# Performance work log

Measured on AMD Instinct MI355X. Metric: run time of the kernel, lower is better.

Reference implementation:

```python
import jax, jax.numpy as jnp
import numpy as np

H, KVH, DH = 16, 4, 64
DIM = 1024
SCALE_BASE = 4096  # context_len
EPS = 1e-6


def rmsnorm(x, g):
    return x * jax.lax.rsqrt(jnp.mean(x * x, axis=-1, keepdims=True) + EPS) * g


def rope_tables(n, dh, dtype):
    inv_freq = 1.0 / (10000.0 ** (jnp.arange(0, dh, 2, dtype=jnp.float32) / dh))
    t = jnp.arange(n, dtype=jnp.float32) * (SCALE_BASE / n)
    freqs = t[:, None] * inv_freq[None, :]          # [n, dh/2]
    emb = jnp.concatenate([freqs, freqs], axis=-1)  # [n, dh]
    return jnp.cos(emb).astype(dtype), jnp.sin(emb).astype(dtype)


def apply_rope(x, cos, sin):
    # x: [b, h, n, dh]; cos/sin: [n, dh]
    x1, x2 = jnp.split(x, 2, axis=-1)
    rot = jnp.concatenate([-x2, x1], axis=-1)
    return x * cos + rot * sin


def setup_inputs() -> dict:
    key = jax.random.key(0)
    ks = jax.random.split(key, 12)
    B, N = 1, 2048
    std = 0.02
    inp = {
        "x": jax.random.normal(ks[0], (B, N, DIM), jnp.float32),
        "a": jax.random.normal(ks[1], (B, N, DIM), jnp.float32),
        "g_x": jnp.ones((DIM,), jnp.float32),
        "g_a": jnp.ones((DIM,), jnp.float32),
        "Wq_x": jax.random.normal(ks[2], (DIM, H * DH), jnp.float32) * std,
        "Wkv_x": jax.random.normal(ks[3], (DIM, 2 * KVH * DH), jnp.float32) * std,
        "Wq_a": jax.random.normal(ks[4], (DIM, H * DH), jnp.float32) * std,
        "Wkv_a": jax.random.normal(ks[5], (DIM, 2 * KVH * DH), jnp.float32) * std,
        "Wout_x": jax.random.normal(ks[6], (H * DH, DIM), jnp.float32) * std,
        "bout_x": jnp.zeros((DIM,), jnp.float32),
        "Wout_a": jax.random.normal(ks[7], (H * DH, DIM), jnp.float32) * std,
        "bout_a": jnp.zeros((DIM,), jnp.float32),
    }
    return inp


def _split_heads(t, h):
    b, n, hd = t.shape
    return t.reshape(b, n, h, hd // h).transpose(0, 2, 1, 3)  # b h n d


def _stream_qkv(s, g, Wq, Wkv):
    s = rmsnorm(s, g)
    q = _split_heads(s @ Wq, H)                 # [b, H, n, DH]
    kv = s @ Wkv
    k, v = jnp.split(kv, 2, axis=-1)
    k = _split_heads(k, KVH)                    # [b, KVH, n, DH]
    v = _split_heads(v, KVH)
    return q, k, v


def reference(x, a, g_x, g_a, Wq_x, Wkv_x, Wq_a, Wkv_a, Wout_x, bout_x, Wout_a, bout_a):
    B, Nx, _ = x.shape
    Na = a.shape[1]
    scale = DH ** -0.5
    r = H // KVH

    q_x, k_x, v_x = _stream_qkv(x, g_x, Wq_x, Wkv_x)
    q_a, k_a, v_a = _stream_qkv(a, g_a, Wq_a, Wkv_a)

    cos_x, sin_x = rope_tables(Nx, DH, x.dtype)
    cos_a, sin_a = rope_tables(Na, DH, a.dtype)
    q_x, k_x = apply_rope(q_x, cos_x, sin_x), apply_rope(k_x, cos_x, sin_x)
    q_a, k_a = apply_rope(q_a, cos_a, sin_a), apply_rope(k_a, cos_a, sin_a)

    # NOTE: original scales q by dim_head**-0.5 AND sdpa scales again -> 1/DH total
    q_x = q_x * scale
    q_a = q_a * scale

    # GQA expansion: einops 'b h n d -> b (r h) n d' == tile heads
    tile = lambda t: jnp.tile(t, (1, r, 1, 1))
    k_x, v_x, k_a, v_a = tile(k_x), tile(v_x), tile(k_a), tile(v_a)

    # pack [a, x] along seq
    q = jnp.concatenate([q_a, q_x], axis=2)
    k = jnp.concatenate([k_a, k_x], axis=2)
    v = jnp.concatenate([v_a, v_x], axis=2)

    scores = jnp.einsum('bhqd,bhkd->bhqk', q, k) * scale  # sdpa's own scale
    attn = jax.nn.softmax(scores, axis=-1)
    out = jnp.einsum('bhqk,bhkd->bhqd', attn, v)          # [b, H, Na+Nx, DH]

    out_a, out_x = out[:, :, :Na], out[:, :, Na:]
    merge = lambda t: t.transpose(0, 2, 1, 3).reshape(B, -1, H * DH)
    out_x = merge(out_x) @ Wout_x + bout_x
    out_a = merge(out_a) @ Wout_a + bout_a
    return out_x, out_a
```

## Files before the change

### kernel.cpp

```cpp
#include <hip/hip_runtime.h>
#include <hip/hip_bf16.h>
#include <stdint.h>
#include <math.h>


#define NSEQ 2048
#define NJ   4096
#define DIMM 1024

typedef __attribute__((ext_vector_type(4))) float f32x4;
typedef __attribute__((ext_vector_type(8))) short bf16x8;
typedef __attribute__((ext_vector_type(4))) short bf16x4;

__device__ __forceinline__ unsigned short f2bf(float f) {
  union { float f; uint32_t u; } v; v.f = f;
  return (unsigned short)((v.u + 0x7FFFu + ((v.u >> 16) & 1u)) >> 16);
}

__device__ __forceinline__ uint32_t pack2bf(float a, float b) {
  __hip_bfloat162 h = __float22bfloat162_rn(float2{a, b});
  union { __hip_bfloat162 h; uint32_t u; } c; c.h = h;
  return c.u;
}

#if defined(__has_builtin)
#if __has_builtin(__builtin_amdgcn_exp2f)
#define FAST_EXP2(x) __builtin_amdgcn_exp2f(x)
#endif
#endif
#ifndef FAST_EXP2
#define FAST_EXP2(x) exp2f(x)
#endif

__device__ __forceinline__ void glds16(const void* g, void* l) {
  __builtin_amdgcn_global_load_lds(
      (const __attribute__((address_space(1))) unsigned int*)g,
      (__attribute__((address_space(3))) unsigned int*)l, 16, 0, 0);
}

#define SYNC_VM(N) do {                                                    \
    asm volatile("s_waitcnt vmcnt(" #N ")" ::: "memory");                  \
    __builtin_amdgcn_sched_barrier(0);                                     \
    __builtin_amdgcn_s_barrier();                                          \
    __builtin_amdgcn_sched_barrier(0);                                     \
  } while (0)

__global__ __launch_bounds__(256) void prep_kernel(
    const float* __restrict__ xa, const float* __restrict__ xx,
    const float* __restrict__ ga, const float* __restrict__ gx,
    const float* __restrict__ wqa, const float* __restrict__ wqx,
    const float* __restrict__ wkva, const float* __restrict__ wkvx,
    const float* __restrict__ woa, const float* __restrict__ wox,
    unsigned short* __restrict__ XN, unsigned short* __restrict__ WQT,
    unsigned short* __restrict__ WKVT, unsigned short* __restrict__ WOT,
    float* __restrict__ cosT, float* __restrict__ sinT) {
  __shared__ float tile[32][33];
  __shared__ float red[4];
  int bid = blockIdx.x, t = threadIdx.x;
  if (bid < 256) {
    int idx = bid * 256 + t;
    int pos = idx >> 5, i = idx & 31;
    double inv = 1.0;
    if (i & 1)  inv *= 0.74989420933245582;
    if (i & 2)  inv *= 0.56234132519034908;
    if (i & 4)  inv *= 0.31622776601683794;
    if (i & 8)  inv *= 0.1;
    if (i & 16) inv *= 0.01;
    double ang = (double)(2 * pos) * inv;
    double rev = ang * 0.15915494309189535;
    rev -= floor(rev);
    float rf = (float)rev;
    float c, s;
    asm("v_cos_f32 %0, %1" : "=v"(c) : "v"(rf));
    asm("v_sin_f32 %0, %1" : "=v"(s) : "v"(rf));
    cosT[idx] = c;
    sinT[idx] = s;
  } else if (bid < 6400) {
    int b = bid - 256;
    int z = b >> 10, yx = b & 1023;
    int n0 = (yx >> 5) * 32, k0 = (yx & 31) * 32;
    int s = z & 1, ty = z >> 1;
    int N = (ty == 1) ? 512 : 1024;
    if (n0 >= N) return;
    const float* src = (z == 0) ? wqa : (z == 1) ? wqx : (z == 2) ? wkva
                     : (z == 3) ? wkvx : (z == 4) ? woa : wox;
    unsigned short* dst = (ty == 0) ? WQT + (size_t)s * 1024 * 1024
                        : (ty == 1) ? WKVT + (size_t)s * 512 * 1024
                                    : WOT + (size_t)s * 1024 * 1024;
    int r = t >> 3, c4 = (t & 7) * 4;
    f32x4 v = *(const f32x4*)(src + (size_t)(k0 + r) * N + n0 + c4);
    tile[r][c4 + 0] = v.x; tile[r][c4 + 1] = v.y;
    tile[r][c4 + 2] = v.z; tile[r][c4 + 3] = v.w;
    __syncthreads();
    int nn = t >> 3, kk = (t & 7) * 4;
    bf16x4 o;
    o.x = (short)f2bf(tile[kk + 0][nn]);
    o.y = (short)f2bf(tile[kk + 1][nn]);
    o.z = (short)f2bf(tile[kk + 2][nn]);
    o.w = (short)f2bf(tile[kk + 3][nn]);
    *(bf16x4*)(dst + (size_t)(n0 + nn) * 1024 + k0 + kk) = o;
  } else {
    int b = bid - 6400;
    int s = b >> 11, row = b & 2047;
    const float* src = (s == 0 ? xa : xx) + (size_t)row * DIMM;
    const float* g = (s == 0 ? ga : gx);
    f32x4 v = *(const f32x4*)(src + t * 4);
    float ss = v.x * v.x + v.y * v.y + v.z * v.z + v.w * v.w;
#pragma unroll
    for (int o = 32; o > 0; o >>= 1) ss += __shfl_xor(ss, o, 64);
    if ((t & 63) == 0) red[t >> 6] = ss;
    __syncthreads();
    float tot = red[0] + red[1] + red[2] + red[3];
    float rs = rsqrtf(tot * (1.0f / DIMM) + 1e-6f);
    f32x4 gv = *(const f32x4*)(g + t * 4);
    bf16x4 o;
    o.x = (short)f2bf(v.x * rs * gv.x);
    o.y = (short)f2bf(v.y * rs * gv.y);
    o.z = (short)f2bf(v.z * rs * gv.z);
    o.w = (short)f2bf(v.w * rs * gv.w);
    *(bf16x4*)(XN + ((size_t)s * NSEQ + row) * DIMM + t * 4) = o;
  }
}

__device__ __forceinline__ void gemm64_mainloop(
    const unsigned short* __restrict__ Ag, const unsigned short* __restrict__ Bg,
    unsigned short* As, unsigned short* Bs, f32x4 acc[2][4]) {
  int t = threadIdx.x;
  int lane = t & 63, wid = t >> 6;
  int wm = (wid >> 1) * 32, wn = (wid & 1) * 64;
  int l15 = lane & 15, quad = lane >> 4;
  int srow = t >> 2, sko = (t & 3) * 8;
  const unsigned short* ga = Ag + (size_t)srow * 1024 + sko;
  const unsigned short* gb = Bg + (size_t)srow * 1024 + sko;
  unsigned short* la = As + t * 8;
  unsigned short* lb = Bs + t * 8;
#pragma unroll
  for (int mi = 0; mi < 2; ++mi)
#pragma unroll
    for (int j = 0; j < 4; ++j) acc[mi][j] = (f32x4){0.f, 0.f, 0.f, 0.f};

#define GQ_STAGE(S, KT) do {                                               \
    int k0_ = (KT) * 32;                                                   \
    glds16(ga + k0_, la + (S) * 2048);                                     \
    glds16(gb + k0_, lb + (S) * 4096);                                     \
    glds16(gb + 64 * 1024 + k0_, lb + (S) * 4096 + 2048);                  \
  } while (0)

#define GQ_COMP(S) do {                                                    \
    bf16x8 af[2], bfr[4];                                                  \
    _Pragma("unroll")                                                      \
    for (int mi = 0; mi < 2; ++mi)                                         \
      af[mi] = *(const bf16x8*)(As + (S) * 2048 + (wm + mi * 16 + l15) * 32 + quad * 8); \
    _Pragma("unroll")                                                      \
    for (int j = 0; j < 4; ++j)                                            \
      bfr[j] = *(const bf16x8*)(Bs + (S) * 4096 + (wn + j * 16 + l15) * 32 + quad * 8); \
    _Pragma("unroll")                                                      \
    for (int mi = 0; mi < 2; ++mi)                                         \
      _Pragma("unroll")                                                    \
      for (int j = 0; j < 4; ++j)                                          \
        acc[mi][j] = __builtin_amdgcn_mfma_f32_16x16x32_bf16(af[mi], bfr[j], acc[mi][j], 0, 0, 0); \
  } while (0)

  GQ_STAGE(0, 0);
  GQ_STAGE(1, 1);
  SYNC_VM(3);
  for (int kq = 0; kq < 32; kq += 4) {
    GQ_STAGE(2, (kq + 2) & 31);
    GQ_COMP(0);
    SYNC_VM(3);
    GQ_STAGE(3, (kq + 3) & 31);
    GQ_COMP(1);
    SYNC_VM(3);
    GQ_STAGE(0, (kq + 4) & 31);
    GQ_COMP(2);
    SYNC_VM(3);
    GQ_STAGE(1, (kq + 5) & 31);
    GQ_COMP(3);
    SYNC_VM(3);
  }
  asm volatile("s_waitcnt vmcnt(0)" ::: "memory");
#undef GQ_STAGE
#undef GQ_COMP
}

__global__ __launch_bounds__(256) void gemm_qkv_kernel(
    const unsigned short* __restrict__ XN, const unsigned short* __restrict__ WQT,
    const unsigned short* __restrict__ WKVT, const float* __restrict__ cosT,
    const float* __restrict__ sinT, unsigned short* __restrict__ QB,
    unsigned short* __restrict__ KB, unsigned short* __restrict__ VT) {
  __shared__ unsigned short As[4 * 2048], Bs[4 * 4096];
  int n0 = blockIdx.x * 128, m0 = blockIdx.y * 64;
  int s = (m0 >= 2048) ? 1 : 0;
  const unsigned short* Ag = XN + (size_t)m0 * 1024;
  const unsigned short* Bg = (n0 < 1024)
      ? WQT + (size_t)s * 1024 * 1024 + (size_t)n0 * 1024
      : WKVT + (size_t)s * 512 * 1024 + (size_t)(n0 - 1024) * 1024;
  f32x4 acc[2][4];
  gemm64_mainloop(Ag, Bg, As, Bs, acc);
  int t = threadIdx.x, lane = t & 63, wid = t >> 6;
  int wm = (wid >> 1) * 32, wn = (wid & 1) * 64;
  int l15 = lane & 15, quad = lane >> 4;
  int coln = n0 + wn;
  if (coln < 1280) {
    bool isq = coln < 1024;
    float sc = isq ? (1.4426950408889634f / 64.0f) : 1.0f;
    unsigned short* dstBase;
    if (isq) dstBase = QB + (size_t)(coln >> 6) * NJ * 64;
    else     dstBase = KB + (size_t)((coln - 1024) >> 6) * NJ * 64;
#pragma unroll
    for (int mi = 0; mi < 2; ++mi)
#pragma unroll
      for (int r = 0; r < 4; ++r) {
        int jr = m0 + wm + mi * 16 + quad * 4 + r;
        int pos = jr & 2047;
#pragma unroll
        for (int jp = 0; jp < 2; ++jp) {
          int i = jp * 16 + l15;
          float c = cosT[pos * 32 + i], sn = sinT[pos * 32 + i];
          float x1 = acc[mi][jp][r], x2 = acc[mi][jp + 2][r];
          dstBase[(size_t)jr * 64 + jp * 16 + l15]      = f2bf((x1 * c - x2 * sn) * sc);
          dstBase[(size_t)jr * 64 + 32 + jp * 16 + l15] = f2bf((x2 * c + x1 * sn) * sc);
        }
      }
  } else {
    int cvb = coln - 1280;
#pragma unroll
    for (int mi = 0; mi < 2; ++mi)
#pragma unroll
      for (int j = 0; j < 4; ++j) {
        int d = cvb + j * 16 + l15;
        int jr0 = m0 + wm + mi * 16 + quad * 4;
        union { bf16x4 v; uint32_t u[2]; } pv;
        pv.u[0] = pack2bf(acc[mi][j][0], acc[mi][j][1]);
        pv.u[1] = pack2bf(acc[mi][j][2], acc[mi][j][3]);
        *(bf16x4*)(VT + (size_t)d * NJ + jr0) = pv.v;
      }
  }
}

__global__ __launch_bounds__(256, 2) void attn_kernel(
    const unsigned short* __restrict__ QB, const unsigned short* __restrict__ KB,
    const unsigned short* __restrict__ VT, unsigned short* __restrict__ AT) {
  __shared__ __align__(16) unsigned short Ks[4][4096];
  __shared__ __align__(16) unsigned short Vs[4][4096];
  int h = blockIdx.y, qt = blockIdx.x;
  int hk = h & 3;
  int t = threadIdx.x, lane = t & 63, w = t >> 6;
  int l15 = lane & 15, quad = lane >> 4;
  int qsel = w >> 1, ksel = w & 1;
  int q0 = qt * 128 + qsel * 64;
  bf16x8 qf[4][2];
#pragma unroll
  for (int mi = 0; mi < 4; ++mi) {
    const unsigned short* qp = QB + ((size_t)h * NJ + q0 + mi * 16 + l15) * 64;
    qf[mi][0] = *(const bf16x8*)(qp + quad * 8);
    qf[mi][1] = *(const bf16x8*)(qp + 32 + quad * 8);
  }
  f32x4 oT[4][4];
  f32x4 oL[4];
#pragma unroll
  for (int mi = 0; mi < 4; ++mi) {
    oL[mi] = (f32x4){0.f, 0.f, 0.f, 0.f};
#pragma unroll
    for (int db = 0; db < 4; ++db) oT[mi][db] = (f32x4){0.f, 0.f, 0.f, 0.f};
  }
  bf16x8 vone;
  {
    short one = (l15 == 0) ? (short)0x3F80 : (short)0;
    vone = (bf16x8){one, one, one, one, one, one, one, one};
  }
  const unsigned short* Kg = KB + (size_t)hk * NJ * 64;
  const unsigned short* Vg = VT + (size_t)hk * 64 * NJ;
  int r1 = t >> 3, cx = t & 7;
  int e1 = r1 & 7;
  int c1 = cx ^ e1;
  int gk1 = 32 * (r1 >> 5) + 8 * ((r1 >> 2) & 3) + 4 * ((r1 >> 4) & 1) + (r1 & 3);
  int r2 = r1 + 32;
  int gk2 = 32 * (r2 >> 5) + 8 * ((r2 >> 2) & 3) + 4 * ((r2 >> 4) & 1) + (r2 & 3);
  const unsigned short* sK1 = Kg + (size_t)gk1 * 64 + c1 * 8;
  const unsigned short* sK2 = Kg + (size_t)gk2 * 64 + c1 * 8;
  const unsigned short* sV1 = Vg + (size_t)r1 * NJ + c1 * 8;
  const unsigned short* sV2 = Vg + (size_t)r2 * NJ + c1 * 8;
  int e = l15 & 7;
  int co0 = (quad ^ e) * 8;
  int co1 = ((4 + quad) ^ e) * 8;
  int cov = (((ksel << 2) | quad) ^ e) * 8;
  const unsigned short* kf0p = &Ks[0][(2 * ksel * 16 + l15) * 64] + co0;
  const unsigned short* kf0q = &Ks[0][(2 * ksel * 16 + l15) * 64] + co1;
  const unsigned short* kf1p = kf0p + 16 * 64;
  const unsigned short* kf1q = kf0q + 16 * 64;
  const unsigned short* vap0 = &Vs[0][(0 * 16 + l15) * 64] + cov;
  const unsigned short* vap1 = &Vs[0][(1 * 16 + l15) * 64] + cov;
  const unsigned short* vap2 = &Vs[0][(2 * 16 + l15) * 64] + cov;
  const unsigned short* vap3 = &Vs[0][(3 * 16 + l15) * 64] + cov;

  f32x4 sxA[4][2], sxB[4][2];
  bf16x8 pb[4];

#define STAGE(S, T) do {                                                   \
    size_t ko_ = (size_t)(T) * 4096;                                       \
    int vo_ = (T) * 64;                                                    \
    glds16(sK1 + ko_, &Ks[S][0] + t * 8);                                  \
    glds16(sK2 + ko_, &Ks[S][2048] + t * 8);                               \
    glds16(sV1 + vo_, &Vs[S][0] + t * 8);                                  \
    glds16(sV2 + vo_, &Vs[S][2048] + t * 8);                               \
  } while (0)

#define QK4(S, SX) do {                                                    \
    bf16x8 k00 = *(const bf16x8*)(kf0p + (S) * 4096);                      \
    bf16x8 k01 = *(const bf16x8*)(kf0q + (S) * 4096);                      \
    bf16x8 k10 = *(const bf16x8*)(kf1p + (S) * 4096);                      \
    bf16x8 k11 = *(const bf16x8*)(kf1q + (S) * 4096);                      \
    _Pragma("unroll")                                                      \
    for (int mi = 0; mi < 4; ++mi) {                                       \
      f32x4 z0 = (f32x4){0.f, 0.f, 0.f, 0.f};                              \
      z0 = __builtin_amdgcn_mfma_f32_16x16x32_bf16(k00, qf[mi][0], z0, 0, 0, 0); \
      z0 = __builtin_amdgcn_mfma_f32_16x16x32_bf16(k01, qf[mi][1], z0, 0, 0, 0); \
      (SX)[mi][0] = z0;                                                    \
      f32x4 z1 = (f32x4){0.f, 0.f, 0.f, 0.f};                              \
      z1 = __builtin_amdgcn_mfma_f32_16x16x32_bf16(k10, qf[mi][0], z1, 0, 0, 0); \
      z1 = __builtin_amdgcn_mfma_f32_16x16x32_bf16(k11, qf[mi][1], z1, 0, 0, 0); \
      (SX)[mi][1] = z1;                                                    \
    }                                                                      \
  } while (0)

#define PHASE_A(SQ, SXN, SXP) do {                                         \
    bf16x8 k00 = *(const bf16x8*)(kf0p + (SQ) * 4096);                     \
    bf16x8 k01 = *(const bf16x8*)(kf0q + (SQ) * 4096);                     \
    bf16x8 k10 = *(const bf16x8*)(kf1p + (SQ) * 4096);                     \
    bf16x8 k11 = *(const bf16x8*)(kf1q + (SQ) * 4096);                     \
    _Pragma("unroll")                                                      \
    for (int mi = 0; mi < 4; ++mi) {                                       \
      f32x4 z0 = (f32x4){0.f, 0.f, 0.f, 0.f};                              \
      z0 = __builtin_amdgcn_mfma_f32_16x16x32_bf16(k00, qf[mi][0], z0, 0, 0, 0); \
      z0 = __builtin_amdgcn_mfma_f32_16x16x32_bf16(k01, qf[mi][1], z0, 0, 0, 0); \
      (SXN)[mi][0] = z0;                                                   \
      f32x4 z1 = (f32x4){0.f, 0.f, 0.f, 0.f};                              \
      z1 = __builtin_amdgcn_mfma_f32_16x16x32_bf16(k10, qf[mi][0], z1, 0, 0, 0); \
      z1 = __builtin_amdgcn_mfma_f32_16x16x32_bf16(k11, qf[mi][1], z1, 0, 0, 0); \
      (SXN)[mi][1] = z1;                                                   \
      union { bf16x8 v; uint32_t u[4]; } pk_;                              \
      pk_.u[0] = pack2bf(FAST_EXP2((SXP)[mi][0][0]), FAST_EXP2((SXP)[mi][0][1])); \
      pk_.u[1] = pack2bf(FAST_EXP2((SXP)[mi][0][2]), FAST_EXP2((SXP)[mi][0][3])); \
      pk_.u[2] = pack2bf(FAST_EXP2((SXP)[mi][1][0]), FAST_EXP2((SXP)[mi][1][1])); \
      pk_.u[3] = pack2bf(FAST_EXP2((SXP)[mi][1][2]), FAST_EXP2((SXP)[mi][1][3])); \
      pb[mi] = pk_.v;                                                      \
    }                                                                      \
  } while (0)

#define PHASE_B(SP) do {                                                   \
    __builtin_amdgcn_s_setprio(1);                                         \
    {                                                                      \
      bf16x8 va0 = *(const bf16x8*)(vap0 + (SP) * 4096);                   \
      bf16x8 va1 = *(const bf16x8*)(vap1 + (SP) * 4096);                   \
      bf16x8 va2 = *(const bf16x8*)(vap2 + (SP) * 4096);                   \
      bf16x8 va3 = *(const bf16x8*)(vap3 + (SP) * 4096);                   \
      _Pragma("unroll")                                                    \
      for (int mi = 0; mi < 4; ++mi) {                                     \
        oT[mi][0] = __builtin_amdgcn_mfma_f32_16x16x32_bf16(va0, pb[mi], oT[mi][0], 0, 0, 0); \
        oT[mi][1] = __builtin_amdgcn_mfma_f32_16x16x32_bf16(va1, pb[mi], oT[mi][1], 0, 0, 0); \
        oT[mi][2] = __builtin_amdgcn_mfma_f32_16x16x32_bf16(va2, pb[mi], oT[mi][2], 0, 0, 0); \
        oT[mi][3] = __builtin_amdgcn_mfma_f32_16x16x32_bf16(va3, pb[mi], oT[mi][3], 0, 0, 0); \
        oL[mi] = __builtin_amdgcn_mfma_f32_16x16x32_bf16(vone, pb[mi], oL[mi], 0, 0, 0); \
      }                                                                    \
    }                                                                      \
    __builtin_amdgcn_s_setprio(0);                                         \
  } while (0)

  STAGE(0, 0);
  STAGE(1, 1);
  STAGE(2, 2);
  SYNC_VM(4);
  QK4(0, sxA);
  for (int P = 0; P < 16; ++P) {
    int tb = 4 * P;
    STAGE(3, (tb + 3) & 63);
    PHASE_A(1, sxB, sxA);
    PHASE_B(0);
    SYNC_VM(4);
    STAGE(0, (tb + 4) & 63);
    PHASE_A(2, sxA, sxB);
    PHASE_B(1);
    SYNC_VM(4);
    STAGE(1, (tb + 5) & 63);
    PHASE_A(3, sxB, sxA);
    PHASE_B(2);
    SYNC_VM(4);
    STAGE(2, (tb + 6) & 63);
    PHASE_A(0, sxA, sxB);
    PHASE_B(3);
    SYNC_VM(4);
  }
  __syncthreads();
#undef STAGE
#undef QK4
#undef PHASE_A
#undef PHASE_B

  float ls[4];
#pragma unroll
  for (int mi = 0; mi < 4; ++mi) {
    float s = oL[mi][0];
    s += __shfl_xor(s, 16, 64);
    s += __shfl_xor(s, 32, 64);
    ls[mi] = s;
  }
  float* xb = (qsel == 0) ? (float*)&Ks[0][0] : (float*)&Vs[0][0];
  float* xl = xb + 64 * 68;
  if (ksel == 1) {
    f32x4* dst = (f32x4*)xb + (size_t)lane * 17;
#pragma unroll
    for (int mi = 0; mi < 4; ++mi)
#pragma unroll
      for (int db = 0; db < 4; ++db) dst[mi * 4 + db] = oT[mi][db];
    float* dl = xl + lane * 4;
#pragma unroll
    for (int mi = 0; mi < 4; ++mi) dl[mi] = ls[mi];
  }
  __syncthreads();
  if (ksel == 0) {
    const f32x4* src = (const f32x4*)xb + (size_t)lane * 17;
    const float* sl = xl + lane * 4;
#pragma unroll
    for (int mi = 0; mi < 4; ++mi) {
      float inv = 1.0f / (ls[mi] + sl[mi]);
      int qrow = q0 + mi * 16 + l15;
#pragma unroll
      for (int db = 0; db < 4; ++db) {
        f32x4 o = oT[mi][db] + src[mi * 4 + db];
        union { bf16x4 v; uint32_t u[2]; } ov;
        ov.u[0] = pack2bf(o[0] * inv, o[1] * inv);
        ov.u[1] = pack2bf(o[2] * inv, o[3] * inv);
        *(bf16x4*)(AT + (size_t)qrow * DIMM + h * 64 + db * 16 + quad * 4) = ov.v;
      }
    }
  }
}

__global__ __launch_bounds__(256) void gemm_out_kernel(
    const unsigned short* __restrict__ AT, const unsigned short* __restrict__ WOT,
    const float* __restrict__ ba, const float* __restrict__ bx,
    float* __restrict__ out) {
  __shared__ unsigned short As[4 * 2048], Bs[4 * 4096];
  int n0 = blockIdx.x * 128, m0 = blockIdx.y * 64;
  int s = (m0 >= 2048) ? 1 : 0;
  const unsigned short* Ag = AT + (size_t)m0 * 1024;
  const unsigned short* Bg = WOT + (size_t)s * 1024 * 1024 + (size_t)n0 * 1024;
  f32x4 acc[2][4];
  gemm64_mainloop(Ag, Bg, As, Bs, acc);
  int t = threadIdx.x, lane = t & 63, wid = t >> 6;
  int wm = (wid >> 1) * 32, wn = (wid & 1) * 64;
  int l15 = lane & 15, quad = lane >> 4;
  const float* bias = s ? bx : ba;
  float* obase = s ? (out + (size_t)(m0 - 2048) * 1024)
                   : (out + (size_t)2048 * 1024 + (size_t)m0 * 1024);
#pragma unroll
  for (int mi = 0; mi < 2; ++mi)
#pragma unroll
    for (int r = 0; r < 4; ++r) {
      int row = wm + mi * 16 + quad * 4 + r;
#pragma unroll
      for (int j = 0; j < 4; ++j) {
        int col = n0 + wn + j * 16 + l15;
        obase[(size_t)row * 1024 + col] = acc[mi][j][r] + bias[col];
      }
    }
}

extern "C" void kernel_launch(void* const* d_in, const int* in_sizes, int n_in,
                              void* d_out, int out_size, void* d_ws, size_t ws_size,
                              hipStream_t stream) {
  const float* x      = (const float*)d_in[0];
  const float* a      = (const float*)d_in[1];
  const float* g_x    = (const float*)d_in[2];
  const float* g_a    = (const float*)d_in[3];
  const float* Wq_x   = (const float*)d_in[4];
  const float* Wkv_x  = (const float*)d_in[5];
  const float* Wq_a   = (const float*)d_in[6];
  const float* Wkv_a  = (const float*)d_in[7];
  const float* Wout_x = (const float*)d_in[8];
  const float* bout_x = (const float*)d_in[9];
  const float* Wout_a = (const float*)d_in[10];
  const float* bout_a = (const float*)d_in[11];
  float* out = (float*)d_out;

  char* ws = (char*)d_ws;
  const size_t MB = 1024 * 1024;
  unsigned short* XN   = (unsigned short*)(ws);
  unsigned short* WQT  = (unsigned short*)(ws + 8 * MB);
  unsigned short* WKVT = (unsigned short*)(ws + 12 * MB);
  unsigned short* WOT  = (unsigned short*)(ws + 14 * MB);
  unsigned short* QB   = (unsigned short*)(ws + 18 * MB);
  unsigned short* KB   = (unsigned short*)(ws + 26 * MB);
  unsigned short* VT   = (unsigned short*)(ws + 28 * MB);
  float* cosT          = (float*)(ws + 30 * MB);
  float* sinT          = (float*)(ws + 30 * MB + 262144);
  unsigned short* AT   = XN;

  prep_kernel<<<dim3(10496), dim3(256), 0, stream>>>(
      a, x, g_a, g_x, Wq_a, Wq_x, Wkv_a, Wkv_x, Wout_a, Wout_x,
      XN, WQT, WKVT, WOT, cosT, sinT);
  gemm_qkv_kernel<<<dim3(12, 64), dim3(256), 0, stream>>>(
      XN, WQT, WKVT, cosT, sinT, QB, KB, VT);
  attn_kernel<<<dim3(32, 16), dim3(256), 0, stream>>>(QB, KB, VT, AT);
  gemm_out_kernel<<<dim3(8, 64), dim3(256), 0, stream>>>(
      AT, WOT, bout_a, bout_x, out);
}
```

Measured before the change: 223.6 us.

## Enlarge QKV GEMM tile to 128x128 and compute RoPE inline

The QKV projection kernel moves from a 64x128 to a 128x128 block tile, with each wave holding a 4x4 grid of MFMA accumulators, and the grid halves in M. This raises data reuse per LDS load. RoPE cos/sin values are now computed on the fly in the epilogue using double-precision angle math, which removes the precomputed table, its prep blocks and its global reads. The cost is more registers, fewer blocks (384 versus 768) to spread across the CUs, and extra double-precision ALU work in the epilogue.

```diff
diff --git a/kernel.cpp b/kernel.cpp
--- a/kernel.cpp
+++ b/kernel.cpp
@@ -45,6 +45,22 @@
     __builtin_amdgcn_sched_barrier(0);                                     \
   } while (0)
 
+__device__ __forceinline__ void rope_cs(int pos, int i, float* c, float* s) {
+  double inv = 1.0;
+  if (i & 1)  inv *= 0.74989420933245582;
+  if (i & 2)  inv *= 0.56234132519034908;
+  if (i & 4)  inv *= 0.31622776601683794;
+  if (i & 8)  inv *= 0.1;
+  if (i & 16) inv *= 0.01;
+  double rev = (double)(2 * pos) * inv * 0.15915494309189535;
+  rev -= floor(rev);
+  float rf = (float)rev;
+  float cc, ss;
+  asm("v_cos_f32 %0, %1" : "=v"(cc) : "v"(rf));
+  asm("v_sin_f32 %0, %1" : "=v"(ss) : "v"(rf));
+  *c = cc; *s = ss;
+}
+
 __global__ __launch_bounds__(256) void prep_kernel(
     const float* __restrict__ xa, const float* __restrict__ xx,
     const float* __restrict__ ga, const float* __restrict__ gx,
@@ -52,31 +68,12 @@
     const float* __restrict__ wkva, const float* __restrict__ wkvx,
     const float* __restrict__ woa, const float* __restrict__ wox,
     unsigned short* __restrict__ XN, unsigned short* __restrict__ WQT,
-    unsigned short* __restrict__ WKVT, unsigned short* __restrict__ WOT,
-    float* __restrict__ cosT, float* __restrict__ sinT) {
+    unsigned short* __restrict__ WKVT, unsigned short* __restrict__ WOT) {
   __shared__ float tile[32][33];
   __shared__ float red[4];
   int bid = blockIdx.x, t = threadIdx.x;
-  if (bid < 256) {
-    int idx = bid * 256 + t;
-    int pos = idx >> 5, i = idx & 31;
-    double inv = 1.0;
-    if (i & 1)  inv *= 0.74989420933245582;
-    if (i & 2)  inv *= 0.56234132519034908;
-    if (i & 4)  inv *= 0.31622776601683794;
-    if (i & 8)  inv *= 0.1;
-    if (i & 16) inv *= 0.01;
-    double ang = (double)(2 * pos) * inv;
-    double rev = ang * 0.15915494309189535;
-    rev -= floor(rev);
-    float rf = (float)rev;
-    float c, s;
-    asm("v_cos_f32 %0, %1" : "=v"(c) : "v"(rf));
-    asm("v_sin_f32 %0, %1" : "=v"(s) : "v"(rf));
-    cosT[idx] = c;
-    sinT[idx] = s;
-  } else if (bid < 6400) {
-    int b = bid - 256;
+  if (bid < 6144) {
+    int b = bid;
     int z = b >> 10, yx = b & 1023;
     int n0 = (yx >> 5) * 32, k0 = (yx & 31) * 32;
     int s = z & 1, ty = z >> 1;
@@ -100,7 +97,7 @@
     o.w = (short)f2bf(tile[kk + 3][nn]);
     *(bf16x4*)(dst + (size_t)(n0 + nn) * 1024 + k0 + kk) = o;
   } else {
-    int b = bid - 6400;
+    int b = bid - 6144;
     int s = b >> 11, row = b & 2047;
     const float* src = (s == 0 ? xa : xx) + (size_t)row * DIMM;
     const float* g = (s == 0 ? ga : gx);
@@ -122,6 +119,115 @@
   }
 }
 
+__global__ __launch_bounds__(256) void gemm_qkv_kernel(
+    const unsigned short* __restrict__ XN, const unsigned short* __restrict__ WQT,
+    const unsigned short* __restrict__ WKVT, unsigned short* __restrict__ QB,
+    unsigned short* __restrict__ KB, unsigned short* __restrict__ VT) {
+  __shared__ unsigned short As[4 * 4096], Bs[4 * 4096];
+  int n0 = blockIdx.x * 128, m0 = blockIdx.y * 128;
+  int s = (m0 >= 2048) ? 1 : 0;
+  const unsigned short* Ag = XN + (size_t)m0 * 1024;
+  const unsigned short* Bg = (n0 < 1024)
+      ? WQT + (size_t)s * 1024 * 1024 + (size_t)n0 * 1024
+      : WKVT + (size_t)s * 512 * 1024 + (size_t)(n0 - 1024) * 1024;
+  int t = threadIdx.x;
+  int lane = t & 63, wid = t >> 6;
+  int wm = (wid >> 1) * 64, wn = (wid & 1) * 64;
+  int l15 = lane & 15, quad = lane >> 4;
+  int srow = t >> 2, sko = (t & 3) * 8;
+  const unsigned short* ga = Ag + (size_t)srow * 1024 + sko;
+  const unsigned short* gb = Bg + (size_t)srow * 1024 + sko;
+  unsigned short* la = As + t * 8;
+  unsigned short* lb = Bs + t * 8;
+  f32x4 acc[4][4];
+#pragma unroll
+  for (int mi = 0; mi < 4; ++mi)
+#pragma unroll
+    for (int j = 0; j < 4; ++j) acc[mi][j] = (f32x4){0.f, 0.f, 0.f, 0.f};
+
+#define GQ_STAGE(S, KT) do {                                               \
+    int k0_ = (KT) * 32;                                                   \
+    glds16(ga + k0_, la + (S) * 4096);                                     \
+    glds16(ga + 64 * 1024 + k0_, la + (S) * 4096 + 2048);                  \
+    glds16(gb + k0_, lb + (S) * 4096);                                     \
+    glds16(gb + 64 * 1024 + k0_, lb + (S) * 4096 + 2048);                  \
+  } while (0)
+
+#define GQ_COMP(S) do {                                                    \
+    bf16x8 af[4], bfr[4];                                                  \
+    _Pragma("unroll")                                                      \
+    for (int mi = 0; mi < 4; ++mi)                                         \
+      af[mi] = *(const bf16x8*)(As + (S) * 4096 + (wm + mi * 16 + l15) * 32 + quad * 8); \
+    _Pragma("unroll")                                                      \
+    for (int j = 0; j < 4; ++j)                                            \
+      bfr[j] = *(const bf16x8*)(Bs + (S) * 4096 + (wn + j * 16 + l15) * 32 + quad * 8); \
+    _Pragma("unroll")                                                      \
+    for (int mi = 0; mi < 4; ++mi)                                         \
+      _Pragma("unroll")                                                    \
+      for (int j = 0; j < 4; ++j)                                          \
+        acc[mi][j] = __builtin_amdgcn_mfma_f32_16x16x32_bf16(af[mi], bfr[j], acc[mi][j], 0, 0, 0); \
+  } while (0)
+
+  GQ_STAGE(0, 0);
+  GQ_STAGE(1, 1);
+  SYNC_VM(4);
+  for (int kq = 0; kq < 32; kq += 4) {
+    GQ_STAGE(2, (kq + 2) & 31);
+    GQ_COMP(0);
+    SYNC_VM(4);
+    GQ_STAGE(3, (kq + 3) & 31);
+    GQ_COMP(1);
+    SYNC_VM(4);
+    GQ_STAGE(0, (kq + 4) & 31);
+    GQ_COMP(2);
+    SYNC_VM(4);
+    GQ_STAGE(1, (kq + 5) & 31);
+    GQ_COMP(3);
+    SYNC_VM(4);
+  }
+  asm volatile("s_waitcnt vmcnt(0)" ::: "memory");
+#undef GQ_STAGE
+#undef GQ_COMP
+
+  int coln = n0 + wn;
+  if (coln < 1280) {
+    bool isq = coln < 1024;
+    float sc = isq ? (1.4426950408889634f / 64.0f) : 1.0f;
+    unsigned short* dstBase;
+    if (isq) dstBase = QB + (size_t)(coln >> 6) * NJ * 64;
+    else     dstBase = KB + (size_t)((coln - 1024) >> 6) * NJ * 64;
+#pragma unroll
+    for (int mi = 0; mi < 4; ++mi)
+#pragma unroll
+      for (int r = 0; r < 4; ++r) {
+        int jr = m0 + wm + mi * 16 + quad * 4 + r;
+        int pos = jr & 2047;
+#pragma unroll
+        for (int jp = 0; jp < 2; ++jp) {
+          int i = jp * 16 + l15;
+          float c, sn;
+          rope_cs(pos, i, &c, &sn);
+          float x1 = acc[mi][jp][r], x2 = acc[mi][jp + 2][r];
+          dstBase[(size_t)jr * 64 + jp * 16 + l15]      = f2bf((x1 * c - x2 * sn) * sc);
+          dstBase[(size_t)jr * 64 + 32 + jp * 16 + l15] = f2bf((x2 * c + x1 * sn) * sc);
+        }
+      }
+  } else {
+    int cvb = coln - 1280;
+#pragma unroll
+    for (int mi = 0; mi < 4; ++mi)
+#pragma unroll
+      for (int j = 0; j < 4; ++j) {
+        int d = cvb + j * 16 + l15;
+        int jr0 = m0 + wm + mi * 16 + quad * 4;
+        union { bf16x4 v; uint32_t u[2]; } pv;
+        pv.u[0] = pack2bf(acc[mi][j][0], acc[mi][j][1]);
+        pv.u[1] = pack2bf(acc[mi][j][2], acc[mi][j][3]);
+        *(bf16x4*)(VT + (size_t)d * NJ + jr0) = pv.v;
+      }
+  }
+}
+
 __device__ __forceinline__ void gemm64_mainloop(
     const unsigned short* __restrict__ Ag, const unsigned short* __restrict__ Bg,
     unsigned short* As, unsigned short* Bs, f32x4 acc[2][4]) {
@@ -139,14 +245,14 @@
 #pragma unroll
     for (int j = 0; j < 4; ++j) acc[mi][j] = (f32x4){0.f, 0.f, 0.f, 0.f};
 
-#define GQ_STAGE(S, KT) do {                                               \
+#define GO_STAGE(S, KT) do {                                               \
     int k0_ = (KT) * 32;                                                   \
     glds16(ga + k0_, la + (S) * 2048);                                     \
     glds16(gb + k0_, lb + (S) * 4096);                                     \
     glds16(gb + 64 * 1024 + k0_, lb + (S) * 4096 + 2048);                  \
   } while (0)
 
-#define GQ_COMP(S) do {                                                    \
+#define GO_COMP(S) do {                                                    \
     bf16x8 af[2], bfr[4];                                                  \
     _Pragma("unroll")                                                      \
     for (int mi = 0; mi < 2; ++mi)                                         \
@@ -161,81 +267,26 @@
         acc[mi][j] = __builtin_amdgcn_mfma_f32_16x16x32_bf16(af[mi], bfr[j], acc[mi][j], 0, 0, 0); \
   } while (0)
 
-  GQ_STAGE(0, 0);
-  GQ_STAGE(1, 1);
+  GO_STAGE(0, 0);
+  GO_STAGE(1, 1);
   SYNC_VM(3);
   for (int kq = 0; kq < 32; kq += 4) {
-    GQ_STAGE(2, (kq + 2) & 31);
-    GQ_COMP(0);
+    GO_STAGE(2, (kq + 2) & 31);
+    GO_COMP(0);
     SYNC_VM(3);
-    GQ_STAGE(3, (kq + 3) & 31);
-    GQ_COMP(1);
+    GO_STAGE(3, (kq + 3) & 31);
+    GO_COMP(1);
     SYNC_VM(3);
-    GQ_STAGE(0, (kq + 4) & 31);
-    GQ_COMP(2);
+    GO_STAGE(0, (kq + 4) & 31);
+    GO_COMP(2);
     SYNC_VM(3);
-    GQ_STAGE(1, (kq + 5) & 31);
-    GQ_COMP(3);
+    GO_STAGE(1, (kq + 5) & 31);
+    GO_COMP(3);
     SYNC_VM(3);
   }
   asm volatile("s_waitcnt vmcnt(0)" ::: "memory");
-#undef GQ_STAGE
-#undef GQ_COMP
-}
-
-__global__ __launch_bounds__(256) void gemm_qkv_kernel(
-    const unsigned short* __restrict__ XN, const unsigned short* __restrict__ WQT,
-    const unsigned short* __restrict__ WKVT, const float* __restrict__ cosT,
-    const float* __restrict__ sinT, unsigned short* __restrict__ QB,
-    unsigned short* __restrict__ KB, unsigned short* __restrict__ VT) {
-  __shared__ unsigned short As[4 * 2048], Bs[4 * 4096];
-  int n0 = blockIdx.x * 128, m0 = blockIdx.y * 64;
-  int s = (m0 >= 2048) ? 1 : 0;
-  const unsigned short* Ag = XN + (size_t)m0 * 1024;
-  const unsigned short* Bg = (n0 < 1024)
-      ? WQT + (size_t)s * 1024 * 1024 + (size_t)n0 * 1024
-      : WKVT + (size_t)s * 512 * 1024 + (size_t)(n0 - 1024) * 1024;
-  f32x4 acc[2][4];
-  gemm64_mainloop(Ag, Bg, As, Bs, acc);
-  int t = threadIdx.x, lane = t & 63, wid = t >> 6;
-  int wm = (wid >> 1) * 32, wn = (wid & 1) * 64;
-  int l15 = lane & 15, quad = lane >> 4;
-  int coln = n0 + wn;
-  if (coln < 1280) {
-    bool isq = coln < 1024;
-    float sc = isq ? (1.4426950408889634f / 64.0f) : 1.0f;
-    unsigned short* dstBase;
-    if (isq) dstBase = QB + (size_t)(coln >> 6) * NJ * 64;
-    else     dstBase = KB + (size_t)((coln - 1024) >> 6) * NJ * 64;
-#pragma unroll
-    for (int mi = 0; mi < 2; ++mi)
-#pragma unroll
-      for (int r = 0; r < 4; ++r) {
-        int jr = m0 + wm + mi * 16 + quad * 4 + r;
-        int pos = jr & 2047;
-#pragma unroll
-        for (int jp = 0; jp < 2; ++jp) {
-          int i = jp * 16 + l15;
-          float c = cosT[pos * 32 + i], sn = sinT[pos * 32 + i];
-          float x1 = acc[mi][jp][r], x2 = acc[mi][jp + 2][r];
-          dstBase[(size_t)jr * 64 + jp * 16 + l15]      = f2bf((x1 * c - x2 * sn) * sc);
-          dstBase[(size_t)jr * 64 + 32 + jp * 16 + l15] = f2bf((x2 * c + x1 * sn) * sc);
-        }
-      }
-  } else {
-    int cvb = coln - 1280;
-#pragma unroll
-    for (int mi = 0; mi < 2; ++mi)
-#pragma unroll
-      for (int j = 0; j < 4; ++j) {
-        int d = cvb + j * 16 + l15;
-        int jr0 = m0 + wm + mi * 16 + quad * 4;
-        union { bf16x4 v; uint32_t u[2]; } pv;
-        pv.u[0] = pack2bf(acc[mi][j][0], acc[mi][j][1]);
-        pv.u[1] = pack2bf(acc[mi][j][2], acc[mi][j][3]);
-        *(bf16x4*)(VT + (size_t)d * NJ + jr0) = pv.v;
-      }
-  }
+#undef GO_STAGE
+#undef GO_COMP
 }
 
 __global__ __launch_bounds__(256, 2) void attn_kernel(
@@ -493,15 +544,13 @@
   unsigned short* QB   = (unsigned short*)(ws + 18 * MB);
   unsigned short* KB   = (unsigned short*)(ws + 26 * MB);
   unsigned short* VT   = (unsigned short*)(ws + 28 * MB);
-  float* cosT          = (float*)(ws + 30 * MB);
-  float* sinT          = (float*)(ws + 30 * MB + 262144);
   unsigned short* AT   = XN;
 
-  prep_kernel<<<dim3(10496), dim3(256), 0, stream>>>(
+  prep_kernel<<<dim3(10240), dim3(256), 0, stream>>>(
       a, x, g_a, g_x, Wq_a, Wq_x, Wkv_a, Wkv_x, Wout_a, Wout_x,
-      XN, WQT, WKVT, WOT, cosT, sinT);
-  gemm_qkv_kernel<<<dim3(12, 64), dim3(256), 0, stream>>>(
-      XN, WQT, WKVT, cosT, sinT, QB, KB, VT);
+      XN, WQT, WKVT, WOT);
+  gemm_qkv_kernel<<<dim3(12, 32), dim3(256), 0, stream>>>(
+      XN, WQT, WKVT, QB, KB, VT);
   attn_kernel<<<dim3(32, 16), dim3(256), 0, stream>>>(QB, KB, VT, AT);
   gemm_out_kernel<<<dim3(8, 64), dim3(256), 0, stream>>>(
       AT, WOT, bout_a, bout_x, out);
```

Result: no change. 222.9 us (-0.3%).
